# Optimization experiments

Hardware: AMD Instinct MI355X
Metric: run time of the kernel (lower is better)

Reference implementation:

```python
import jax, jax.numpy as jnp
import numpy as np

NUM_HEADS = 16
EPS = 1e-12  # matches F.normalize eps


def _l2norm(x):
    return x / jnp.maximum(jnp.linalg.norm(x, axis=-1, keepdims=True), EPS)


def setup_inputs() -> dict:
    key = jax.random.key(0)
    ks = jax.random.split(key, 8)
    B, S, E, M = 2, 2048, 1024, 16384
    sc = 0.02
    return {
        "hidden_states": jax.random.normal(ks[0], (B, S, E), jnp.float32),
        "memory_keys": jax.random.normal(ks[1], (M, E), jnp.float32),
        "memory_values": jax.random.normal(ks[2], (M, E), jnp.float32),
        "Wq": jax.random.normal(ks[3], (E, E), jnp.float32) * sc,
        "bq": jnp.zeros((E,), jnp.float32),
        "Wk": jax.random.normal(ks[4], (E, E), jnp.float32) * sc,
        "bk": jnp.zeros((E,), jnp.float32),
        "Wv": jax.random.normal(ks[5], (E, E), jnp.float32) * sc,
        "bv": jnp.zeros((E,), jnp.float32),
        "Wo": jax.random.normal(ks[6], (E, E), jnp.float32) * sc,
        "bo": jnp.zeros((E,), jnp.float32),
        "top_k": 8,
    }


def reference(hidden_states, memory_keys, memory_values, Wq, bq, Wk, bk, Wv, bv, Wo, bo, top_k):
    B, S, E = hidden_states.shape
    H = NUM_HEADS
    hd = E // H
    scale = 1.0 / jnp.sqrt(jnp.float32(hd))

    def heads(x):  # [B,S,E] -> [B,H,S,hd]
        return x.reshape(B, S, H, hd).transpose(0, 2, 1, 3)

    q = heads(hidden_states @ Wq.T + bq)
    k = heads(hidden_states @ Wk.T + bk)
    v = heads(hidden_states @ Wv.T + bv)

    # self-attention scores [B,H,S,S]
    scores = jnp.einsum('bhqd,bhkd->bhqk', q, k) * scale

    # memory retrieval: cosine sim of raw hidden states vs memory keys
    qn = _l2norm(hidden_states)           # [B,S,E]
    kn = _l2norm(memory_keys)             # [M,E]
    sims = jnp.einsum('bse,me->bsm', qn, kn)   # [B,S,M]
    top_vals, top_idx = jax.lax.top_k(sims, top_k)  # [B,S,K]
    retrieved = memory_values[top_idx]    # [B,S,K,E] gather
    ret_h = retrieved.reshape(B, S, top_k, H, hd).transpose(0, 3, 1, 2, 4)  # [B,H,S,K,hd]

    # concat retrieval similarities as extra attention columns, re-softmax
    mem_scores = jnp.broadcast_to(top_vals[:, None, :, :], (B, H, S, top_k))
    ext = jnp.concatenate([scores, mem_scores], axis=-1)   # [B,H,S,S+K]
    probs = jax.nn.softmax(ext, axis=-1)

    ctx = jnp.einsum('bhqk,bhkd->bhqd', probs[..., :S], v)
    ctx = ctx + jnp.einsum('bhqk,bhqkd->bhqd', probs[..., S:], ret_h)

    ctx = ctx.transpose(0, 2, 1, 3).reshape(B, S, E)
    return ctx @ Wo.T + bo
```

## Files before the change

### kernel.cpp

```cpp
#include <hip/hip_runtime.h>
#include <math.h>

#define R_TOT 4096
#define E_DIM 1024
#define M_DIM 16384
#define H_NUM 16
#define HD    64
#define SEQ   2048
#define BATCH 2
#define TOPK  8
#define MIDK  16
#define NCHUNK 16
#define SCHUNK 1024
#define CANDS  32

typedef __attribute__((ext_vector_type(8))) short short8_t;
typedef __attribute__((ext_vector_type(4))) float f32x4;

__device__ inline unsigned short f2bf(float x) {
  unsigned u = __float_as_uint(x);
  u = (u + 0x7fff + ((u >> 16) & 1)) >> 16;
  return (unsigned short)u;
}
__device__ inline float bf2f(unsigned short h) {
  return __uint_as_float(((unsigned)h) << 16);
}

#define GLDS16(gp, lp) __builtin_amdgcn_global_load_lds( \
    (const __attribute__((address_space(1))) void*)(gp), \
    (__attribute__((address_space(3))) void*)(lp), 16, 0, 0)

__global__ __launch_bounds__(256) void norm_bf16_kernel(const float* __restrict__ X,
                                                        unsigned short* __restrict__ Y,
                                                        unsigned short* __restrict__ Yraw,
                                                        float* __restrict__ rinv_out) {
  int row = blockIdx.x;
  int tid = threadIdx.x;
  const float4* xr = (const float4*)(X + (size_t)row * E_DIM);
  float4 v = xr[tid];
  float s = v.x*v.x + v.y*v.y + v.z*v.z + v.w*v.w;
  #pragma unroll
  for (int off = 32; off; off >>= 1) s += __shfl_down(s, off, 64);
  __shared__ float wsum[4];
  if ((tid & 63) == 0) wsum[tid >> 6] = s;
  __syncthreads();
  float tot = wsum[0] + wsum[1] + wsum[2] + wsum[3];
  float rinv = 1.0f / fmaxf(sqrtf(tot), 1e-12f);
  if (tid == 0) rinv_out[row] = rinv;
  ushort4 o;
  o.x = f2bf(v.x * rinv); o.y = f2bf(v.y * rinv);
  o.z = f2bf(v.z * rinv); o.w = f2bf(v.w * rinv);
  ((ushort4*)(Y + (size_t)row * E_DIM))[tid] = o;
  if (Yraw) {
    ushort4 o2;
    o2.x = f2bf(v.x); o2.y = f2bf(v.y); o2.z = f2bf(v.z); o2.w = f2bf(v.w);
    ((ushort4*)(Yraw + (size_t)row * E_DIM))[tid] = o2;
  }
}

__global__ __launch_bounds__(256) void cast_bf16_kernel(const float* __restrict__ X,
                                                        unsigned short* __restrict__ Y, int n4) {
  int i = blockIdx.x * 256 + threadIdx.x;
  if (i < n4) {
    float4 v = ((const float4*)X)[i];
    ushort4 o;
    o.x = f2bf(v.x); o.y = f2bf(v.y); o.z = f2bf(v.z); o.w = f2bf(v.w);
    ((ushort4*)Y)[i] = o;
  }
}

template<int OUT_BF16>
__device__ __forceinline__ void gemm_tile_body(
    const unsigned short* __restrict__ Ab, const unsigned short* __restrict__ Bb,
    const float* __restrict__ bias, void* __restrict__ C, int N,
    int bm, int bn, char* pool) {
  short* Ap = (short*)pool;
  short* Bp = (short*)(pool + 16384);
  int tid = threadIdx.x;
  int wave = tid >> 6, lane = tid & 63;
  int wr = wave >> 1, wc = wave & 1;
  int li8 = lane >> 3;
  int gslot = (lane & 7) ^ li8;

  f32x4 acc[4][4];
  #pragma unroll
  for (int i = 0; i < 4; ++i)
    #pragma unroll
    for (int j = 0; j < 4; ++j)
      acc[i][j] = (f32x4){0.f, 0.f, 0.f, 0.f};

  for (int k0 = 0; k0 < E_DIM; k0 += 64) {
    #pragma unroll
    for (int s4 = 0; s4 < 8; ++s4) {
      int s = wave * 8 + s4;
      const unsigned short* gp;
      if (s < 16) {
        int r = s * 8 + li8;
        gp = Ab + (size_t)(bm + r) * E_DIM + k0 + gslot * 8;
      } else {
        int r = (s - 16) * 8 + li8;
        gp = Bb + (size_t)(bn + r) * E_DIM + k0 + gslot * 8;
      }
      GLDS16(gp, pool + s * 1024);
    }
    __syncthreads();
    #pragma unroll
    for (int ks = 0; ks < 2; ++ks) {
      short8_t af[4], bf[4];
      int kslot = ks * 4 + (lane >> 4);
      #pragma unroll
      for (int mi = 0; mi < 4; ++mi) {
        int r = wr * 64 + mi * 16 + (lane & 15);
        af[mi] = *(const short8_t*)(Ap + r * 64 + ((kslot ^ (r & 7)) * 8));
      }
      #pragma unroll
      for (int ni = 0; ni < 4; ++ni) {
        int r = wc * 64 + ni * 16 + (lane & 15);
        bf[ni] = *(const short8_t*)(Bp + r * 64 + ((kslot ^ (r & 7)) * 8));
      }
      #pragma unroll
      for (int mi = 0; mi < 4; ++mi)
        #pragma unroll
        for (int ni = 0; ni < 4; ++ni)
          acc[mi][ni] = __builtin_amdgcn_mfma_f32_16x16x32_bf16(af[mi], bf[ni], acc[mi][ni], 0, 0, 0);
    }
    __syncthreads();
  }
  #pragma unroll
  for (int mi = 0; mi < 4; ++mi) {
    #pragma unroll
    for (int ni = 0; ni < 4; ++ni) {
      int col = bn + wc * 64 + ni * 16 + (lane & 15);
      float bv = bias[col];
      #pragma unroll
      for (int r = 0; r < 4; ++r) {
        int row = bm + wr * 64 + mi * 16 + (lane >> 4) * 4 + r;
        float v = acc[mi][ni][r] + bv;
        if (OUT_BF16)
          ((unsigned short*)C)[(size_t)row * N + col] = f2bf(v);
        else
          ((float*)C)[(size_t)row * N + col] = v;
      }
    }
  }
}

__global__ __launch_bounds__(256) void mfma_gemm_out(
    const unsigned short* __restrict__ Ab, const unsigned short* __restrict__ Bb,
    const float* __restrict__ bias, float* __restrict__ C) {
  __shared__ __align__(16) char pool[32768];
  gemm_tile_body<0>(Ab, Bb, bias, C, E_DIM, blockIdx.x * 128, blockIdx.y * 128, pool);
}

__global__ __launch_bounds__(256) void mfma_gemm_qkv(
    const unsigned short* __restrict__ hb,
    const unsigned short* __restrict__ wq, const unsigned short* __restrict__ wk,
    const unsigned short* __restrict__ wv,
    const float* __restrict__ bq, const float* __restrict__ bk, const float* __restrict__ bv,
    unsigned short* __restrict__ q_b, unsigned short* __restrict__ k_b,
    unsigned short* __restrict__ v_b) {
  __shared__ __align__(16) char pool[32768];
  int bn_g = blockIdx.y * 128;
  int sel = bn_g >> 10;
  int bn = bn_g & 1023;
  const unsigned short* Bb = (sel == 0) ? wq : (sel == 1) ? wk : wv;
  const float* bias = (sel == 0) ? bq : (sel == 1) ? bk : bv;
  unsigned short* C = (sel == 0) ? q_b : (sel == 1) ? k_b : v_b;
  gemm_tile_body<1>(hb, Bb, bias, C, E_DIM, blockIdx.x * 128, bn, pool);
}

__global__ __launch_bounds__(256) void vtrans_kernel(const unsigned short* __restrict__ vb,
                                                     unsigned short* __restrict__ vT) {
  int st = blockIdx.x;
  int bh = blockIdx.y;
  int b = bh >> 4, h = bh & 15;
  __shared__ short T[64][72];
  int tid = threadIdx.x;
  #pragma unroll
  for (int it = 0; it < 2; ++it) {
    int idx = tid + it * 256;
    int r = idx >> 3, sl = idx & 7;
    short8_t v = *(const short8_t*)(vb + ((size_t)(b * SEQ + st * 64 + r)) * E_DIM + h * HD + sl * 8);
    *(short8_t*)&T[r][sl * 8] = v;
  }
  __syncthreads();
  int d = tid >> 2, sp = (tid & 3) * 16;
  short8_t o0, o1;
  #pragma unroll
  for (int u = 0; u < 8; ++u) o0[u] = T[sp + u][d];
  #pragma unroll
  for (int u = 0; u < 8; ++u) o1[u] = T[sp + 8 + u][d];
  size_t base = ((size_t)bh * HD + d) * SEQ + st * 64 + sp;
  *(short8_t*)(vT + base) = o0;
  *(short8_t*)(vT + base + 8) = o1;
}

#define SPITCH 132
#define NSTEP (SCHUNK / 128 * 16)

__global__ __launch_bounds__(512) void sims_topk_kernel(
    const unsigned short* __restrict__ Hn, const unsigned short* __restrict__ MKn,
    float* __restrict__ cand_v, int* __restrict__ cand_i) {
  __shared__ __align__(16) char pool[65536 + 128 * SPITCH * 2];
  short* Sp = (short*)(pool + 65536);

  int bm = blockIdx.x * 128;
  int chunk = blockIdx.y;
  int tid = threadIdx.x;
  int wave = tid >> 6, lane = tid & 63;
  int wr = wave >> 2, wc = wave & 3;
  int srow = tid >> 2, sl = tid & 3;
  int li8 = lane >> 3;
  int gslot = (lane & 7) ^ li8;

  float tv[TOPK]; int ti[TOPK];
  #pragma unroll
  for (int u = 0; u < TOPK; ++u) { tv[u] = -INFINITY; ti[u] = 0; }

  auto STAGE = [&](int d, int t) {
    int sub = t >> 4;
    int k0 = (t & 15) * 64;
    int bn = chunk * SCHUNK + sub * 128;
    #pragma unroll
    for (int s4 = 0; s4 < 4; ++s4) {
      int s = wave * 4 + s4;
      const unsigned short* gp;
      if (s < 16) {
        int r = s * 8 + li8;
        gp = Hn + (size_t)(bm + r) * E_DIM + k0 + gslot * 8;
      } else {
        int r = (s - 16) * 8 + li8;
        gp = MKn + (size_t)(bn + r) * E_DIM + k0 + gslot * 8;
      }
      GLDS16(gp, pool + d * 32768 + s * 1024);
    }
  };

  f32x4 acc[4][2];
  #pragma unroll
  for (int i = 0; i < 4; ++i)
    #pragma unroll
    for (int j = 0; j < 2; ++j)
      acc[i][j] = (f32x4){0.f, 0.f, 0.f, 0.f};

  STAGE(0, 0);

  for (int t = 0; t < NSTEP; ++t) {
    int cur = t & 1;
    if (t + 1 < NSTEP) {
      STAGE(1 - cur, t + 1);
      asm volatile("s_waitcnt vmcnt(4)" ::: "memory");
    } else {
      asm volatile("s_waitcnt vmcnt(0)" ::: "memory");
    }
    __builtin_amdgcn_s_barrier();
    __builtin_amdgcn_sched_barrier(0);

    short* Ap = (short*)(pool + cur * 32768);
    short* Bp = (short*)(pool + cur * 32768 + 16384);
    #pragma unroll
    for (int ks = 0; ks < 2; ++ks) {
      short8_t af[4], bf[2];
      int kslot = ks * 4 + (lane >> 4);
      #pragma unroll
      for (int mi = 0; mi < 4; ++mi) {
        int r = wr * 64 + mi * 16 + (lane & 15);
        af[mi] = *(const short8_t*)(Ap + r * 64 + ((kslot ^ (r & 7)) * 8));
      }
      #pragma unroll
      for (int ni = 0; ni < 2; ++ni) {
        int r = wc * 32 + ni * 16 + (lane & 15);
        bf[ni] = *(const short8_t*)(Bp + r * 64 + ((kslot ^ (r & 7)) * 8));
      }
      #pragma unroll
      for (int mi = 0; mi < 4; ++mi)
        #pragma unroll
        for (int ni = 0; ni < 2; ++ni)
          acc[mi][ni] = __builtin_amdgcn_mfma_f32_16x16x32_bf16(af[mi], bf[ni], acc[mi][ni], 0, 0, 0);
    }
    __builtin_amdgcn_sched_barrier(0);
    __builtin_amdgcn_s_barrier();

    if ((t & 15) == 15) {
      int bn = chunk * SCHUNK + (t >> 4) * 128;
      #pragma unroll
      for (int mi = 0; mi < 4; ++mi) {
        #pragma unroll
        for (int ni = 0; ni < 2; ++ni) {
          int scol = wc * 32 + ni * 16 + (lane & 15);
          #pragma unroll
          for (int r = 0; r < 4; ++r) {
            int srw = wr * 64 + mi * 16 + (lane >> 4) * 4 + r;
            Sp[srw * SPITCH + scol] = (short)f2bf(acc[mi][ni][r]);
          }
          acc[mi][ni] = (f32x4){0.f, 0.f, 0.f, 0.f};
        }
      }
      __syncthreads();
      #pragma unroll
      for (int u4 = 0; u4 < 8; ++u4) {
        const short* p = Sp + srow * SPITCH + sl * 32 + u4 * 4;
        short4 v4 = *(const short4*)p;
        short vv[4] = {v4.x, v4.y, v4.z, v4.w};
        #pragma unroll
        for (int j = 0; j < 4; ++j) {
          float v = bf2f((unsigned short)vv[j]);
          if (v > tv[0]) {
            int idx = bn + sl * 32 + u4 * 4 + j;
            int p_ = 0;
            #pragma unroll
            for (int q = 1; q < TOPK; ++q)
              if (v > tv[q]) { tv[q-1] = tv[q]; ti[q-1] = ti[q]; p_ = q; }
            tv[p_] = v; ti[p_] = idx;
          }
        }
      }
      __syncthreads();
    }
  }
  size_t base = (((size_t)(bm + srow)) * NCHUNK + chunk) * CANDS + sl * TOPK;
  #pragma unroll
  for (int u = 0; u < TOPK; ++u) { cand_v[base + u] = tv[u]; cand_i[base + u] = ti[u]; }
}

__global__ __launch_bounds__(64) void merge_topk_kernel(
    const float* __restrict__ cand_v, const int* __restrict__ cand_i,
    int* __restrict__ mid_i) {
  int row = blockIdx.x;
  int lane = threadIdx.x;
  size_t base = (size_t)row * (NCHUNK * CANDS);
  float v[8]; int id[8];
  #pragma unroll
  for (int u = 0; u < 8; ++u) {
    v[u]  = cand_v[base + lane*8 + u];
    id[u] = cand_i[base + lane*8 + u];
  }
  for (int t = 0; t < MIDK; ++t) {
    float bvv = v[0]; int bu = 0;
    #pragma unroll
    for (int u = 1; u < 8; ++u) if (v[u] > bvv) { bvv = v[u]; bu = u; }
    float mv = bvv; int ml = lane;
    #pragma unroll
    for (int off = 32; off; off >>= 1) {
      float ov = __shfl_down(mv, off, 64);
      int   ol = __shfl_down(ml, off, 64);
      if (ov > mv) { mv = ov; ml = ol; }
    }
    ml = __shfl(ml, 0, 64);
    if (lane == ml) {
      mid_i[(size_t)row * MIDK + t] = id[bu];
      v[bu] = -INFINITY;
    }
  }
}

__global__ __launch_bounds__(256) void refine_kernel(
    const float* __restrict__ hidden, const float* __restrict__ mkeys,
    const float* __restrict__ rinvH, const float* __restrict__ rinvK,
    const int* __restrict__ mid_i,
    float* __restrict__ top_v, int* __restrict__ top_i) {
  int row = blockIdx.x;
  int tid = threadIdx.x;
  int wave = tid >> 6, lane = tid & 63;
  __shared__ float hrow[E_DIM];
  __shared__ float rv[MIDK];
  __shared__ int   ri[MIDK];
  ((float4*)hrow)[tid] = ((const float4*)(hidden + (size_t)row * E_DIM))[tid];
  __syncthreads();
  float rh = rinvH[row];
  for (int c = wave; c < MIDK; c += 4) {
    int idx = mid_i[(size_t)row * MIDK + c];
    const float* kp = mkeys + (size_t)idx * E_DIM;
    float s = 0.f;
    #pragma unroll
    for (int rr = 0; rr < 4; ++rr) {
      float4 kv = *(const float4*)(kp + rr * 256 + lane * 4);
      float4 hv = *(const float4*)(hrow + rr * 256 + lane * 4);
      s += hv.x*kv.x + hv.y*kv.y + hv.z*kv.z + hv.w*kv.w;
    }
    #pragma unroll
    for (int off = 32; off; off >>= 1) s += __shfl_down(s, off, 64);
    if (lane == 0) { rv[c] = s * rh * rinvK[idx]; ri[c] = idx; }
  }
  __syncthreads();
  if (tid == 0) {
    bool used[MIDK] = {};
    #pragma unroll
    for (int t = 0; t < TOPK; ++t) {
      float best = -INFINITY; int bi = -1; int bidx = 0x7fffffff;
      for (int c = 0; c < MIDK; ++c) {
        if (used[c]) continue;
        if (rv[c] > best || (rv[c] == best && ri[c] < bidx)) {
          best = rv[c]; bi = c; bidx = ri[c];
        }
      }
      used[bi] = true;
      top_v[(size_t)row * TOPK + t] = best;
      top_i[(size_t)row * TOPK + t] = bidx;
    }
  }
}

__global__ __launch_bounds__(256) void flash_mfma_kernel(
    const unsigned short* __restrict__ qb, const unsigned short* __restrict__ kb,
    const unsigned short* __restrict__ vT, const float* __restrict__ MV,
    const float* __restrict__ top_v, const int* __restrict__ top_i,
    unsigned short* __restrict__ ctx) {
  __shared__ __align__(16) char pool[32768];
  short* Kp = (short*)pool;
  short* Vp = (short*)(pool + 8192);
  int qt = blockIdx.x;
  int bh = blockIdx.y;
  int b = bh >> 4, h = bh & 15;
  int tid = threadIdx.x;
  int wave = tid >> 6, lane = tid & 63;
  int g = lane >> 4, c = lane & 15;
  int li8 = lane >> 3;
  int gslot = (lane & 7) ^ li8;
  short* Pw = (short*)(pool + 16384 + wave * 4096);
  const float scale = 0.125f;

  short8_t aQ[2][2];
  #pragma unroll
  for (int mi = 0; mi < 2; ++mi)
    #pragma unroll
    for (int ks = 0; ks < 2; ++ks) {
      size_t row = (size_t)b * SEQ + qt * 128 + wave * 32 + mi * 16 + c;
      aQ[mi][ks] = *(const short8_t*)(qb + row * E_DIM + h * HD + (ks * 4 + g) * 8);
    }

  f32x4 oa[2][4];
  #pragma unroll
  for (int mi = 0; mi < 2; ++mi)
    #pragma unroll
    for (int nd = 0; nd < 4; ++nd)
      oa[mi][nd] = (f32x4){0.f, 0.f, 0.f, 0.f};
  float m_[2][4], l_[2][4];
  #pragma unroll
  for (int mi = 0; mi < 2; ++mi)
    #pragma unroll
    for (int r = 0; r < 4; ++r) { m_[mi][r] = -INFINITY; l_[mi][r] = 0.f; }

  for (int kv0 = 0; kv0 < SEQ; kv0 += 64) {
    #pragma unroll
    for (int j = 0; j < 4; ++j) {
      int s = wave * 4 + j;
      const unsigned short* gp;
      if (s < 8) {
        int r = s * 8 + li8;
        gp = kb + ((size_t)(b * SEQ + kv0 + r)) * E_DIM + h * HD + gslot * 8;
      } else {
        int d = (s - 8) * 8 + li8;
        gp = vT + ((size_t)(bh * HD + d)) * SEQ + kv0 + gslot * 8;
      }
      GLDS16(gp, pool + s * 1024);
    }
    __syncthreads();

    f32x4 sa[2][4];
    #pragma unroll
    for (int mi = 0; mi < 2; ++mi)
      #pragma unroll
      for (int ni = 0; ni < 4; ++ni)
        sa[mi][ni] = (f32x4){0.f, 0.f, 0.f, 0.f};
    #pragma unroll
    for (int ks = 0; ks < 2; ++ks) {
      short8_t bK[4];
      #pragma unroll
      for (int ni = 0; ni < 4; ++ni) {
        int r = ni * 16 + c;
        bK[ni] = *(const short8_t*)(Kp + r * 64 + (((ks * 4 + g) ^ (r & 7)) * 8));
      }
      #pragma unroll
      for (int mi = 0; mi < 2; ++mi)
        #pragma unroll
        for (int ni = 0; ni < 4; ++ni)
          sa[mi][ni] = __builtin_amdgcn_mfma_f32_16x16x32_bf16(aQ[mi][ks], bK[ni], sa[mi][ni], 0, 0, 0);
    }
    #pragma unroll
    for (int mi = 0; mi < 2; ++mi)
      #pragma unroll
      for (int ni = 0; ni < 4; ++ni)
        #pragma unroll
        for (int r = 0; r < 4; ++r)
          sa[mi][ni][r] *= scale;
    float fsc[2][4];
    #pragma unroll
    for (int mi = 0; mi < 2; ++mi)
      #pragma unroll
      for (int r = 0; r < 4; ++r) {
        float m0 = fmaxf(fmaxf(sa[mi][0][r], sa[mi][1][r]), fmaxf(sa[mi][2][r], sa[mi][3][r]));
        #pragma unroll
        for (int off = 1; off < 16; off <<= 1) m0 = fmaxf(m0, __shfl_xor(m0, off, 64));
        float mn = fmaxf(m_[mi][r], m0);
        fsc[mi][r] = __expf(m_[mi][r] - mn);
        m_[mi][r] = mn;
      }
    #pragma unroll
    for (int mi = 0; mi < 2; ++mi)
      #pragma unroll
      for (int nd = 0; nd < 4; ++nd)
        #pragma unroll
        for (int r = 0; r < 4; ++r)
          oa[mi][nd][r] *= fsc[mi][r];
    #pragma unroll
    for (int mi = 0; mi < 2; ++mi)
      #pragma unroll
      for (int r = 0; r < 4; ++r) {
        float ps = 0.f;
        #pragma unroll
        for (int ni = 0; ni < 4; ++ni) {
          float p = __expf(sa[mi][ni][r] - m_[mi][r]);
          sa[mi][ni][r] = p;
          ps += p;
        }
        #pragma unroll
        for (int off = 1; off < 16; off <<= 1) ps += __shfl_xor(ps, off, 64);
        l_[mi][r] = l_[mi][r] * fsc[mi][r] + ps;
      }
    #pragma unroll
    for (int mi = 0; mi < 2; ++mi)
      #pragma unroll
      for (int ni = 0; ni < 4; ++ni)
        #pragma unroll
        for (int r = 0; r < 4; ++r) {
          int ql = mi * 16 + g * 4 + r;
          int slot = (ni * 2 + (c >> 3)) ^ (ql & 7);
          Pw[ql * 64 + slot * 8 + (c & 7)] = (short)f2bf(sa[mi][ni][r]);
        }
    #pragma unroll
    for (int ks = 0; ks < 2; ++ks) {
      short8_t aP[2], bV[4];
      #pragma unroll
      for (int mi = 0; mi < 2; ++mi) {
        int ql = mi * 16 + c;
        aP[mi] = *(const short8_t*)(Pw + ql * 64 + (((ks * 4 + g) ^ (ql & 7)) * 8));
      }
      #pragma unroll
      for (int nd = 0; nd < 4; ++nd) {
        int dr = nd * 16 + c;
        bV[nd] = *(const short8_t*)(Vp + dr * 64 + (((ks * 4 + g) ^ (dr & 7)) * 8));
      }
      #pragma unroll
      for (int mi = 0; mi < 2; ++mi)
        #pragma unroll
        for (int nd = 0; nd < 4; ++nd)
          oa[mi][nd] = __builtin_amdgcn_mfma_f32_16x16x32_bf16(aP[mi], bV[nd], oa[mi][nd], 0, 0, 0);
    }
    __syncthreads();
  }

  #pragma unroll
  for (int mi = 0; mi < 2; ++mi)
    #pragma unroll
    for (int r = 0; r < 4; ++r) {
      size_t row = (size_t)b * SEQ + qt * 128 + wave * 32 + mi * 16 + g * 4 + r;
      const float* tvp = top_v + row * TOPK;
      const int*   tip = top_i + row * TOPK;
      float lg[TOPK];
      float mmax = m_[mi][r];
      #pragma unroll
      for (int j = 0; j < TOPK; ++j) { lg[j] = tvp[j]; mmax = fmaxf(mmax, lg[j]); }
      float f = __expf(m_[mi][r] - mmax);
      float l = l_[mi][r] * f;
      #pragma unroll
      for (int nd = 0; nd < 4; ++nd) oa[mi][nd][r] *= f;
      #pragma unroll
      for (int j = 0; j < TOPK; ++j) {
        float p = __expf(lg[j] - mmax);
        l += p;
        const float* mvp = MV + (size_t)tip[j] * E_DIM + h * HD + c;
        #pragma unroll
        for (int nd = 0; nd < 4; ++nd)
          oa[mi][nd][r] = fmaf(p, mvp[nd * 16], oa[mi][nd][r]);
      }
      float inv = 1.0f / l;
      #pragma unroll
      for (int nd = 0; nd < 4; ++nd)
        ctx[row * E_DIM + h * HD + nd * 16 + c] = f2bf(oa[mi][nd][r] * inv);
    }
}

extern "C" void kernel_launch(void* const* d_in, const int* in_sizes, int n_in,
                              void* d_out, int out_size, void* d_ws, size_t ws_size,
                              hipStream_t stream) {
  (void)in_sizes; (void)n_in; (void)out_size; (void)ws_size;
  const float* hidden = (const float*)d_in[0];
  const float* mkeys  = (const float*)d_in[1];
  const float* mvals  = (const float*)d_in[2];
  const float* Wq = (const float*)d_in[3];
  const float* bq = (const float*)d_in[4];
  const float* Wk = (const float*)d_in[5];
  const float* bk = (const float*)d_in[6];
  const float* Wv = (const float*)d_in[7];
  const float* bv = (const float*)d_in[8];
  const float* Wo = (const float*)d_in[9];
  const float* bo = (const float*)d_in[10];

  char* ws = (char*)d_ws;
  float* cand_v = (float*)ws;                                  ws += (size_t)R_TOT * NCHUNK * CANDS * 4;
  int*   cand_i = (int*)ws;                                    ws += (size_t)R_TOT * NCHUNK * CANDS * 4;
  int*   mid_i  = (int*)ws;                                    ws += (size_t)R_TOT * MIDK * 4;
  float* top_v  = (float*)ws;                                  ws += (size_t)R_TOT * TOPK * 4;
  int*   top_i  = (int*)ws;                                    ws += (size_t)R_TOT * TOPK * 4;
  float* rinvH  = (float*)ws;                                  ws += (size_t)R_TOT * 4;
  float* rinvK  = (float*)ws;                                  ws += (size_t)M_DIM * 4;
  unsigned short* Hn   = (unsigned short*)ws;                  ws += (size_t)R_TOT * E_DIM * 2;
  unsigned short* MKn  = (unsigned short*)ws;                  ws += (size_t)M_DIM * E_DIM * 2;
  unsigned short* hb   = (unsigned short*)ws;                  ws += (size_t)R_TOT * E_DIM * 2;
  unsigned short* wqb  = (unsigned short*)ws;                  ws += (size_t)E_DIM * E_DIM * 2;
  unsigned short* wkb  = (unsigned short*)ws;                  ws += (size_t)E_DIM * E_DIM * 2;
  unsigned short* wvb  = (unsigned short*)ws;                  ws += (size_t)E_DIM * E_DIM * 2;
  unsigned short* wob  = (unsigned short*)ws;                  ws += (size_t)E_DIM * E_DIM * 2;
  unsigned short* q_b  = (unsigned short*)ws;                  ws += (size_t)R_TOT * E_DIM * 2;
  unsigned short* k_b  = (unsigned short*)ws;                  ws += (size_t)R_TOT * E_DIM * 2;
  unsigned short* v_b  = (unsigned short*)ws;                  ws += (size_t)R_TOT * E_DIM * 2;
  unsigned short* vTb  = (unsigned short*)ws;                  ws += (size_t)R_TOT * E_DIM * 2;
  unsigned short* ctxb = (unsigned short*)ws;                  ws += (size_t)R_TOT * E_DIM * 2;

  norm_bf16_kernel<<<dim3(R_TOT), 256, 0, stream>>>(hidden, Hn, hb, rinvH);
  norm_bf16_kernel<<<dim3(M_DIM), 256, 0, stream>>>(mkeys, MKn, (unsigned short*)nullptr, rinvK);

  int n4w = E_DIM * E_DIM / 4;
  cast_bf16_kernel<<<dim3(n4w / 256), 256, 0, stream>>>(Wq, wqb, n4w);
  cast_bf16_kernel<<<dim3(n4w / 256), 256, 0, stream>>>(Wk, wkb, n4w);
  cast_bf16_kernel<<<dim3(n4w / 256), 256, 0, stream>>>(Wv, wvb, n4w);
  cast_bf16_kernel<<<dim3(n4w / 256), 256, 0, stream>>>(Wo, wob, n4w);

  mfma_gemm_qkv<<<dim3(R_TOT / 128, 3 * E_DIM / 128), 256, 0, stream>>>(
      hb, wqb, wkb, wvb, bq, bk, bv, q_b, k_b, v_b);

  vtrans_kernel<<<dim3(SEQ / 64, BATCH * H_NUM), 256, 0, stream>>>(v_b, vTb);

  sims_topk_kernel<<<dim3(R_TOT / 128, NCHUNK), 512, 0, stream>>>(Hn, MKn, cand_v, cand_i);
  merge_topk_kernel<<<dim3(R_TOT), 64, 0, stream>>>(cand_v, cand_i, mid_i);
  refine_kernel<<<dim3(R_TOT), 256, 0, stream>>>(hidden, mkeys, rinvH, rinvK, mid_i, top_v, top_i);

  flash_mfma_kernel<<<dim3(SEQ / 128, BATCH * H_NUM), 256, 0, stream>>>(
      q_b, k_b, vTb, mvals, top_v, top_i, ctxb);

  mfma_gemm_out<<<dim3(R_TOT / 128, E_DIM / 128), 256, 0, stream>>>(ctxb, wob, bo, (float*)d_out);
}
```

Measured before the change: 575.0 us.

## Enlarge sims_topk tile to 256 query rows with 4x4 MFMA per wave

The similarity/top-k kernel now covers 256 hidden rows per block instead of 128, and each wave computes a 64x64 output tile instead of 64x32. Each memory-key tile loaded into LDS is therefore reused across twice as many query rows, which halves global traffic for the key matrix and raises MFMA work per LDS load. The top-k scan runs in two passes over the shared score buffer, one per 128-row half, with extra barriers. LDS use grows to about 130KB, register pressure rises with 16 accumulators, and the grid shrinks to 256 blocks, which may hurt occupancy and wave scheduling.

```diff
diff --git a/kernel.cpp b/kernel.cpp
--- a/kernel.cpp
+++ b/kernel.cpp
@@ -201,46 +201,48 @@
 __global__ __launch_bounds__(512) void sims_topk_kernel(
     const unsigned short* __restrict__ Hn, const unsigned short* __restrict__ MKn,
     float* __restrict__ cand_v, int* __restrict__ cand_i) {
-  __shared__ __align__(16) char pool[65536 + 128 * SPITCH * 2];
-  short* Sp = (short*)(pool + 65536);
-
-  int bm = blockIdx.x * 128;
+  __shared__ __align__(16) char pool[98304 + 128 * SPITCH * 2];
+  short* Sp = (short*)(pool + 98304);
+
+  int bm = blockIdx.x * 256;
   int chunk = blockIdx.y;
   int tid = threadIdx.x;
   int wave = tid >> 6, lane = tid & 63;
-  int wr = wave >> 2, wc = wave & 3;
+  int wr = wave >> 1, wc = wave & 1;
   int srow = tid >> 2, sl = tid & 3;
   int li8 = lane >> 3;
   int gslot = (lane & 7) ^ li8;
 
-  float tv[TOPK]; int ti[TOPK];
-  #pragma unroll
-  for (int u = 0; u < TOPK; ++u) { tv[u] = -INFINITY; ti[u] = 0; }
+  float tv[2][TOPK]; int ti[2][TOPK];
+  #pragma unroll
+  for (int p = 0; p < 2; ++p)
+    #pragma unroll
+    for (int u = 0; u < TOPK; ++u) { tv[p][u] = -INFINITY; ti[p][u] = 0; }
 
   auto STAGE = [&](int d, int t) {
     int sub = t >> 4;
     int k0 = (t & 15) * 64;
     int bn = chunk * SCHUNK + sub * 128;
     #pragma unroll
-    for (int s4 = 0; s4 < 4; ++s4) {
-      int s = wave * 4 + s4;
+    for (int s4 = 0; s4 < 6; ++s4) {
+      int s = wave * 6 + s4;
       const unsigned short* gp;
-      if (s < 16) {
+      if (s < 32) {
         int r = s * 8 + li8;
         gp = Hn + (size_t)(bm + r) * E_DIM + k0 + gslot * 8;
       } else {
-        int r = (s - 16) * 8 + li8;
+        int r = (s - 32) * 8 + li8;
         gp = MKn + (size_t)(bn + r) * E_DIM + k0 + gslot * 8;
       }
-      GLDS16(gp, pool + d * 32768 + s * 1024);
+      GLDS16(gp, pool + d * 49152 + s * 1024);
     }
   };
 
-  f32x4 acc[4][2];
+  f32x4 acc[4][4];
   #pragma unroll
   for (int i = 0; i < 4; ++i)
     #pragma unroll
-    for (int j = 0; j < 2; ++j)
+    for (int j = 0; j < 4; ++j)
       acc[i][j] = (f32x4){0.f, 0.f, 0.f, 0.f};
 
   STAGE(0, 0);
@@ -249,18 +251,18 @@
     int cur = t & 1;
     if (t + 1 < NSTEP) {
       STAGE(1 - cur, t + 1);
-      asm volatile("s_waitcnt vmcnt(4)" ::: "memory");
+      asm volatile("s_waitcnt vmcnt(6)" ::: "memory");
     } else {
       asm volatile("s_waitcnt vmcnt(0)" ::: "memory");
     }
     __builtin_amdgcn_s_barrier();
     __builtin_amdgcn_sched_barrier(0);
 
-    short* Ap = (short*)(pool + cur * 32768);
-    short* Bp = (short*)(pool + cur * 32768 + 16384);
+    short* Ap = (short*)(pool + cur * 49152);
+    short* Bp = (short*)(pool + cur * 49152 + 32768);
     #pragma unroll
     for (int ks = 0; ks < 2; ++ks) {
-      short8_t af[4], bf[2];
+      short8_t af[4], bf[4];
       int kslot = ks * 4 + (lane >> 4);
       #pragma unroll
       for (int mi = 0; mi < 4; ++mi) {
@@ -268,14 +270,14 @@
         af[mi] = *(const short8_t*)(Ap + r * 64 + ((kslot ^ (r & 7)) * 8));
       }
       #pragma unroll
-      for (int ni = 0; ni < 2; ++ni) {
-        int r = wc * 32 + ni * 16 + (lane & 15);
+      for (int ni = 0; ni < 4; ++ni) {
+        int r = wc * 64 + ni * 16 + (lane & 15);
         bf[ni] = *(const short8_t*)(Bp + r * 64 + ((kslot ^ (r & 7)) * 8));
       }
       #pragma unroll
       for (int mi = 0; mi < 4; ++mi)
         #pragma unroll
-        for (int ni = 0; ni < 2; ++ni)
+        for (int ni = 0; ni < 4; ++ni)
           acc[mi][ni] = __builtin_amdgcn_mfma_f32_16x16x32_bf16(af[mi], bf[ni], acc[mi][ni], 0, 0, 0);
     }
     __builtin_amdgcn_sched_barrier(0);
@@ -284,43 +286,51 @@
     if ((t & 15) == 15) {
       int bn = chunk * SCHUNK + (t >> 4) * 128;
       #pragma unroll
-      for (int mi = 0; mi < 4; ++mi) {
-        #pragma unroll
-        for (int ni = 0; ni < 2; ++ni) {
-          int scol = wc * 32 + ni * 16 + (lane & 15);
+      for (int p = 0; p < 2; ++p) {
+        if ((wr >> 1) == p) {
           #pragma unroll
-          for (int r = 0; r < 4; ++r) {
-            int srw = wr * 64 + mi * 16 + (lane >> 4) * 4 + r;
-            Sp[srw * SPITCH + scol] = (short)f2bf(acc[mi][ni][r]);
-          }
-          acc[mi][ni] = (f32x4){0.f, 0.f, 0.f, 0.f};
-        }
-      }
-      __syncthreads();
-      #pragma unroll
-      for (int u4 = 0; u4 < 8; ++u4) {
-        const short* p = Sp + srow * SPITCH + sl * 32 + u4 * 4;
-        short4 v4 = *(const short4*)p;
-        short vv[4] = {v4.x, v4.y, v4.z, v4.w};
-        #pragma unroll
-        for (int j = 0; j < 4; ++j) {
-          float v = bf2f((unsigned short)vv[j]);
-          if (v > tv[0]) {
-            int idx = bn + sl * 32 + u4 * 4 + j;
-            int p_ = 0;
+          for (int mi = 0; mi < 4; ++mi) {
             #pragma unroll
-            for (int q = 1; q < TOPK; ++q)
-              if (v > tv[q]) { tv[q-1] = tv[q]; ti[q-1] = ti[q]; p_ = q; }
-            tv[p_] = v; ti[p_] = idx;
+            for (int ni = 0; ni < 4; ++ni) {
+              int scol = wc * 64 + ni * 16 + (lane & 15);
+              #pragma unroll
+              for (int r = 0; r < 4; ++r) {
+                int srw = (wr & 1) * 64 + mi * 16 + (lane >> 4) * 4 + r;
+                Sp[srw * SPITCH + scol] = (short)f2bf(acc[mi][ni][r]);
+              }
+              acc[mi][ni] = (f32x4){0.f, 0.f, 0.f, 0.f};
+            }
           }
         }
-      }
-      __syncthreads();
-    }
-  }
-  size_t base = (((size_t)(bm + srow)) * NCHUNK + chunk) * CANDS + sl * TOPK;
-  #pragma unroll
-  for (int u = 0; u < TOPK; ++u) { cand_v[base + u] = tv[u]; cand_i[base + u] = ti[u]; }
+        __syncthreads();
+        #pragma unroll
+        for (int u4 = 0; u4 < 8; ++u4) {
+          const short* pp = Sp + srow * SPITCH + sl * 32 + u4 * 4;
+          short4 v4 = *(const short4*)pp;
+          short vv[4] = {v4.x, v4.y, v4.z, v4.w};
+          #pragma unroll
+          for (int j = 0; j < 4; ++j) {
+            float v = bf2f((unsigned short)vv[j]);
+            if (v > tv[p][0]) {
+              int idx = bn + sl * 32 + u4 * 4 + j;
+              int p_ = 0;
+              #pragma unroll
+              for (int q = 1; q < TOPK; ++q)
+                if (v > tv[p][q]) { tv[p][q-1] = tv[p][q]; ti[p][q-1] = ti[p][q]; p_ = q; }
+              tv[p][p_] = v; ti[p][p_] = idx;
+            }
+          }
+        }
+        __syncthreads();
+      }
+    }
+  }
+  #pragma unroll
+  for (int p = 0; p < 2; ++p) {
+    size_t base = (((size_t)(bm + p * 128 + srow)) * NCHUNK + chunk) * CANDS + sl * TOPK;
+    #pragma unroll
+    for (int u = 0; u < TOPK; ++u) { cand_v[base + u] = tv[p][u]; cand_i[base + u] = ti[p][u]; }
+  }
 }
 
 __global__ __launch_bounds__(64) void merge_topk_kernel(
@@ -632,7 +642,7 @@
 
   vtrans_kernel<<<dim3(SEQ / 64, BATCH * H_NUM), 256, 0, stream>>>(v_b, vTb);
 
-  sims_topk_kernel<<<dim3(R_TOT / 128, NCHUNK), 512, 0, stream>>>(Hn, MKn, cand_v, cand_i);
+  sims_topk_kernel<<<dim3(R_TOT / 256, NCHUNK), 512, 0, stream>>>(Hn, MKn, cand_v, cand_i);
   merge_topk_kernel<<<dim3(R_TOT), 64, 0, stream>>>(cand_v, cand_i, mid_i);
   refine_kernel<<<dim3(R_TOT), 256, 0, stream>>>(hidden, mkeys, rinvH, rinvK, mid_i, top_v, top_i);
 
```

Result: slower. 807.2 us (+40.4%).
